# Performance work log

Measured on AMD Instinct MI355X. Metric: run time of the kernel, lower is better.

Reference implementation:

```python
import jax, jax.numpy as jnp
import numpy as np

B = 1024      # total windows (batch*windows_per_image)
W = 7         # window_size
T = W * W     # tokens per window = 49
C = 256       # scaled_emb_dim = emb_dim * 2**level
H = 8         # heads
D = C // H    # head_dim = 32
NUM_POS = 2 * W - 1


def _relative_pos():
    coords = np.arange(W)
    coords = np.stack(np.meshgrid(coords, coords, indexing='ij')).reshape(2, -1)
    rp = coords[:, :, None] - coords[:, None, :] + (W - 1)
    return jnp.asarray(rp, dtype=jnp.int32)  # (2, T, T)


def setup_inputs() -> dict:
    key = jax.random.key(0)
    ks = jax.random.split(key, 12)
    s = 0.02
    return {
        'x': jax.random.normal(ks[0], (B, T, C), dtype=jnp.float32),
        'relative_pos': _relative_pos(),
        'bias_table': jax.random.truncated_normal(ks[1], -2.0, 2.0, (H, NUM_POS, NUM_POS), dtype=jnp.float32) * s,
        'wq': jax.random.normal(ks[2], (C, H, D), dtype=jnp.float32) / np.sqrt(C),
        'bq': jnp.zeros((H, D), dtype=jnp.float32),
        'wk': jax.random.normal(ks[3], (C, H, D), dtype=jnp.float32) / np.sqrt(C),
        'bk': jnp.zeros((H, D), dtype=jnp.float32),
        'wv': jax.random.normal(ks[4], (C, H, D), dtype=jnp.float32) / np.sqrt(C),
        'bv': jnp.zeros((H, D), dtype=jnp.float32),
        'wo': jax.random.normal(ks[5], (H, D, C), dtype=jnp.float32) / np.sqrt(C),
        'bo': jnp.zeros((C,), dtype=jnp.float32),
        'dw': jax.random.normal(ks[6], (C, C), dtype=jnp.float32) / np.sqrt(C),
        'db': jnp.zeros((C,), dtype=jnp.float32),
    }


def reference(x, relative_pos, bias_table, wq, bq, wk, bk, wv, bv, wo, bo, dw, db):
    # QKV projections (flax DenseGeneral with bias)
    q = jnp.einsum('btc,chd->bthd', x, wq) + bq  # (B,T,H,D)
    k = jnp.einsum('btc,chd->bthd', x, wk) + bk
    v = jnp.einsum('btc,chd->bthd', x, wv) + bv

    # gathered relative position bias: (H, T, T)
    bias = bias_table[:, relative_pos[0], relative_pos[1]]

    # attention logits with query scaling (flax dot_product_attention)
    q = q / jnp.sqrt(jnp.asarray(D, dtype=q.dtype))
    logits = jnp.einsum('bqhd,bkhd->bhqk', q, k) + bias[None]
    attn = jax.nn.softmax(logits, axis=-1)

    out = jnp.einsum('bhqk,bkhd->bqhd', attn, v)
    y = jnp.einsum('bqhd,hdc->bqc', out, wo) + bo  # attention out projection
    y = jnp.einsum('btc,cf->btf', y, dw) + db      # trailing Dense(scaled_emb_dim)
    return y
```

## Files before the change

kernel.cpp:

```cpp
#include <hip/hip_runtime.h>
#include <stdint.h>

#define T 49
#define CCH 256
#define NH 8
#define DH 32

typedef __bf16 bf16x8 __attribute__((ext_vector_type(8)));
typedef float f32x4 __attribute__((ext_vector_type(4)));

static __device__ __forceinline__ unsigned short f2bf(float f){
  uint32_t u = __builtin_bit_cast(uint32_t, f);
  u = u + 0x7fffu + ((u >> 16) & 1u);
  return (unsigned short)(u >> 16);
}
static __device__ __forceinline__ float bf2f(unsigned short h){
  return __builtin_bit_cast(float, ((uint32_t)h) << 16);
}
static __device__ __forceinline__ f32x4 mfma16(bf16x8 a, bf16x8 b, f32x4 c){
  return __builtin_amdgcn_mfma_f32_16x16x32_bf16(a, b, c, 0, 0, 0);
}
#define SWZ(row) ((((row) & 7) << 4))


__global__ void prep_wqkvT(const float* __restrict__ wq, const float* __restrict__ wk,
                           const float* __restrict__ wv, unsigned short* __restrict__ out){
  int bk = blockIdx.x;
  int p = bk >> 8, kk = bk & 255;
  int n = threadIdx.x;
  const float* w = (p == 0) ? wq : (p == 1 ? wk : wv);
  float scl = (p == 0) ? 0.17677669529663687f : 1.0f;
  out[(size_t)(p * 256 + n) * 256 + kk] = f2bf(w[kk * 256 + n] * scl);
}

__global__ void prep_wodT(const float* __restrict__ wo, const float* __restrict__ dw,
                          unsigned short* __restrict__ out){
  int hd = blockIdx.x;
  int c = threadIdx.x;
  float s = 0.f;
  for (int cp = 0; cp < 256; ++cp) s = fmaf(wo[hd * 256 + cp], dw[cp * 256 + c], s);
  out[(size_t)c * 256 + hd] = f2bf(s);
}

__global__ void prep_misc(const int* __restrict__ rp, const float* __restrict__ btab,
                          const float* __restrict__ bq, const float* __restrict__ bk,
                          const float* __restrict__ bv, const float* __restrict__ bo,
                          const float* __restrict__ dwm, const float* __restrict__ db,
                          unsigned short* __restrict__ biasT, float* __restrict__ bqkv,
                          float* __restrict__ bod){
  int t = threadIdx.x;
  if (blockIdx.x == 0){
    for (int idx = t; idx < 768; idx += 256){
      int p = idx >> 8, n = idx & 255;
      float v = (p == 0) ? bq[n] * 0.17677669529663687f : (p == 1 ? bk[n] : bv[n]);
      bqkv[idx] = v;
    }
    float s = db[t];
    for (int cp = 0; cp < 256; ++cp) s = fmaf(bo[cp], dwm[cp * 256 + t], s);
    bod[t] = s;
  } else {
    int h = blockIdx.x - 1;
    for (int idx = t; idx < 4096; idx += 256){
      int j = idx >> 6, i = idx & 63;
      float v;
      if (j >= T) v = -1e30f;
      else if (i >= T) v = 0.f;
      else {
        int r0 = rp[i * 49 + j];
        int r1 = rp[2401 + i * 49 + j];
        v = btab[h * 169 + r0 * 13 + r1];
      }
      biasT[(size_t)(h * 64 + j) * 64 + i] = f2bf(v);
    }
  }
}

__launch_bounds__(512, 2)
__global__ void wmsa_main(const float* __restrict__ x,
                          const unsigned short* __restrict__ wqkvT,
                          const unsigned short* __restrict__ wodT,
                          const unsigned short* __restrict__ biasT,
                          const float* __restrict__ bqkv,
                          const float* __restrict__ bod,
                          float* __restrict__ y){
  __shared__ unsigned short xs[64 * 256];
  __shared__ unsigned short qs[8 * 64 * 40];
  __shared__ unsigned short ksh[8 * 64 * 40];
  __shared__ unsigned short vts[8 * 32 * 64];

  const int b    = blockIdx.x;
  const int tid  = threadIdx.x;
  const int h    = tid >> 6;
  const int lane = tid & 63;
  const int g    = lane >> 4;
  const int lo   = lane & 15;
  char* xs_c = (char*)xs;

  const float* xb = x + (size_t)b * T * CCH;
  for (int idx = tid; idx < 64 * 64; idx += 512){
    int row = idx >> 6, c4 = idx & 63;
    float4 v = make_float4(0.f, 0.f, 0.f, 0.f);
    if (row < T) v = reinterpret_cast<const float4*>(xb)[row * 64 + c4];
    uint32_t w0 = (uint32_t)f2bf(v.x) | ((uint32_t)f2bf(v.y) << 16);
    uint32_t w1 = (uint32_t)f2bf(v.z) | ((uint32_t)f2bf(v.w) << 16);
    *reinterpret_cast<uint2*>(xs_c + row * 512 + ((c4 * 8) ^ SWZ(row))) = make_uint2(w0, w1);
  }
  __syncthreads();

  f32x4 acc[4][6];
  #pragma unroll
  for (int mt = 0; mt < 4; ++mt)
    #pragma unroll
    for (int s = 0; s < 6; ++s) acc[mt][s] = f32x4{0.f, 0.f, 0.f, 0.f};

  for (int kt = 0; kt < 8; ++kt){
    bf16x8 a[4];
    #pragma unroll
    for (int mt = 0; mt < 4; ++mt){
      int row = 16 * mt + lo;
      a[mt] = *reinterpret_cast<const bf16x8*>(xs_c + row * 512 + ((kt * 64 + 16 * g) ^ SWZ(row)));
    }
    #pragma unroll
    for (int s = 0; s < 6; ++s){
      int p = s >> 1, nt = s & 1;
      int nrow = p * 256 + h * 32 + nt * 16 + lo;
      bf16x8 bfr = *reinterpret_cast<const bf16x8*>(wqkvT + (size_t)nrow * 256 + kt * 32 + 8 * g);
      #pragma unroll
      for (int mt = 0; mt < 4; ++mt) acc[mt][s] = mfma16(a[mt], bfr, acc[mt][s]);
    }
  }
  #pragma unroll
  for (int s = 0; s < 6; ++s){
    int p = s >> 1, nt = s & 1;
    int d = nt * 16 + lo;
    float bias = bqkv[p * 256 + h * 32 + d];
    #pragma unroll
    for (int mt = 0; mt < 4; ++mt){
      f32x4 t = acc[mt][s];
      if (p < 2){
        unsigned short* dst = (p == 0 ? qs : ksh) + h * 2560;
        #pragma unroll
        for (int r = 0; r < 4; ++r)
          dst[(16 * mt + 4 * g + r) * 40 + d] = f2bf(t[0 + r] + bias);
      } else {
        uint32_t w0 = (uint32_t)f2bf(t[0] + bias) | ((uint32_t)f2bf(t[1] + bias) << 16);
        uint32_t w1 = (uint32_t)f2bf(t[2] + bias) | ((uint32_t)f2bf(t[3] + bias) << 16);
        *reinterpret_cast<uint2*>((char*)vts + h * 4096 + d * 128 + ((mt * 32 + g * 8) ^ SWZ(d)))
            = make_uint2(w0, w1);
      }
    }
  }
  __syncthreads();

  const char* qb = (const char*)qs + h * 5120;
  const char* kb = (const char*)ksh + h * 5120;
  bf16x8 ak[4], bq_[4];
  #pragma unroll
  for (int tt = 0; tt < 4; ++tt){
    int row = 16 * tt + lo;
    ak[tt]  = *reinterpret_cast<const bf16x8*>(kb + row * 80 + 16 * g);
    bq_[tt] = *reinterpret_cast<const bf16x8*>(qb + row * 80 + 16 * g);
  }
  f32x4 lacc[4][4];
  #pragma unroll
  for (int mt = 0; mt < 4; ++mt)
    #pragma unroll
    for (int nt = 0; nt < 4; ++nt)
      lacc[mt][nt] = mfma16(ak[mt], bq_[nt], f32x4{0.f, 0.f, 0.f, 0.f});

  #pragma unroll
  for (int mt = 0; mt < 4; ++mt)
    #pragma unroll
    for (int nt = 0; nt < 4; ++nt)
      #pragma unroll
      for (int r = 0; r < 4; ++r){
        int j = 16 * mt + 4 * g + r, i = 16 * nt + lo;
        lacc[mt][nt][r] += bf2f(biasT[(size_t)(h * 64 + j) * 64 + i]);
      }

  float rs[4];
  uint32_t pw[4][4][2];
  #pragma unroll
  for (int nt = 0; nt < 4; ++nt){
    float m = -3.0e38f;
    #pragma unroll
    for (int mt = 0; mt < 4; ++mt)
      #pragma unroll
      for (int r = 0; r < 4; ++r) m = fmaxf(m, lacc[mt][nt][r]);
    m = fmaxf(m, __shfl_xor(m, 16, 64));
    m = fmaxf(m, __shfl_xor(m, 32, 64));
    float ssum = 0.f;
    #pragma unroll
    for (int mt = 0; mt < 4; ++mt)
      #pragma unroll
      for (int r = 0; r < 4; ++r){
        float pv = exp2f((lacc[mt][nt][r] - m) * 1.4426950408889634f);
        lacc[mt][nt][r] = pv;
        ssum += pv;
      }
    ssum += __shfl_xor(ssum, 16, 64);
    ssum += __shfl_xor(ssum, 32, 64);
    rs[nt] = 1.f / ssum;
    #pragma unroll
    for (int mt = 0; mt < 4; ++mt){
      pw[mt][nt][0] = (uint32_t)f2bf(lacc[mt][nt][0]) | ((uint32_t)f2bf(lacc[mt][nt][1]) << 16);
      pw[mt][nt][1] = (uint32_t)f2bf(lacc[mt][nt][2]) | ((uint32_t)f2bf(lacc[mt][nt][3]) << 16);
    }
  }

  const char* vb = (const char*)vts + h * 4096;
  f32x4 oacc[2][4];
  #pragma unroll
  for (int mt = 0; mt < 2; ++mt)
    #pragma unroll
    for (int nt = 0; nt < 4; ++nt) oacc[mt][nt] = f32x4{0.f, 0.f, 0.f, 0.f};

  const int src_lo = lo + 32 * (g & 1);
  const int src_hi = src_lo + 16;
  #pragma unroll
  for (int kt = 0; kt < 2; ++kt){
    bf16x8 av[2];
    #pragma unroll
    for (int mt = 0; mt < 2; ++mt){
      int row = 16 * mt + lo;
      av[mt] = *reinterpret_cast<const bf16x8*>(vb + row * 128 + ((kt * 64 + 16 * g) ^ SWZ(row)));
    }
    #pragma unroll
    for (int nt = 0; nt < 4; ++nt){
      uint32_t a0 = (uint32_t)__shfl((int)pw[2 * kt][nt][0], src_lo, 64);
      uint32_t a1 = (uint32_t)__shfl((int)pw[2 * kt][nt][1], src_lo, 64);
      uint32_t a2 = (uint32_t)__shfl((int)pw[2 * kt][nt][0], src_hi, 64);
      uint32_t a3 = (uint32_t)__shfl((int)pw[2 * kt][nt][1], src_hi, 64);
      uint32_t b0 = (uint32_t)__shfl((int)pw[2 * kt + 1][nt][0], src_lo, 64);
      uint32_t b1 = (uint32_t)__shfl((int)pw[2 * kt + 1][nt][1], src_lo, 64);
      uint32_t b2 = (uint32_t)__shfl((int)pw[2 * kt + 1][nt][0], src_hi, 64);
      uint32_t b3 = (uint32_t)__shfl((int)pw[2 * kt + 1][nt][1], src_hi, 64);
      uint4 fu = (g < 2) ? make_uint4(a0, a1, a2, a3) : make_uint4(b0, b1, b2, b3);
      bf16x8 pf = __builtin_bit_cast(bf16x8, fu);
      #pragma unroll
      for (int mt = 0; mt < 2; ++mt) oacc[mt][nt] = mfma16(av[mt], pf, oacc[mt][nt]);
    }
  }
  #pragma unroll
  for (int nt = 0; nt < 4; ++nt){
    int i = 16 * nt + lo;
    float r0 = rs[nt];
    #pragma unroll
    for (int mt = 0; mt < 2; ++mt){
      f32x4 t = oacc[mt][nt];
      uint32_t w0 = (uint32_t)f2bf(t[0] * r0) | ((uint32_t)f2bf(t[1] * r0) << 16);
      uint32_t w1 = (uint32_t)f2bf(t[2] * r0) | ((uint32_t)f2bf(t[3] * r0) << 16);
      *reinterpret_cast<uint2*>(xs_c + i * 512 + ((h * 64 + mt * 32 + g * 8) ^ SWZ(i)))
          = make_uint2(w0, w1);
    }
  }
  __syncthreads();

  f32x4 facc[4][2];
  #pragma unroll
  for (int mt = 0; mt < 4; ++mt)
    #pragma unroll
    for (int nt = 0; nt < 2; ++nt) facc[mt][nt] = f32x4{0.f, 0.f, 0.f, 0.f};

  for (int kt = 0; kt < 8; ++kt){
    bf16x8 a[4];
    #pragma unroll
    for (int mt = 0; mt < 4; ++mt){
      int row = 16 * mt + lo;
      a[mt] = *reinterpret_cast<const bf16x8*>(xs_c + row * 512 + ((kt * 64 + 16 * g) ^ SWZ(row)));
    }
    #pragma unroll
    for (int nt = 0; nt < 2; ++nt){
      int crow = h * 32 + nt * 16 + lo;
      bf16x8 bfr = *reinterpret_cast<const bf16x8*>(wodT + (size_t)crow * 256 + kt * 32 + 8 * g);
      #pragma unroll
      for (int mt = 0; mt < 4; ++mt) facc[mt][nt] = mfma16(a[mt], bfr, facc[mt][nt]);
    }
  }
  #pragma unroll
  for (int nt = 0; nt < 2; ++nt){
    int c = h * 32 + nt * 16 + lo;
    float bd = bod[c];
    #pragma unroll
    for (int mt = 0; mt < 4; ++mt)
      #pragma unroll
      for (int r = 0; r < 4; ++r){
        int i = 16 * mt + 4 * g + r;
        if (i < T) y[((size_t)b * T + i) * CCH + c] = facc[mt][nt][r] + bd;
      }
  }
}

extern "C" void kernel_launch(void* const* d_in, const int* in_sizes, int n_in,
                              void* d_out, int out_size, void* d_ws, size_t ws_size,
                              hipStream_t stream){
  const float* x    = (const float*)d_in[0];
  const int*   rp   = (const int*)d_in[1];
  const float* btab = (const float*)d_in[2];
  const float* wq   = (const float*)d_in[3];
  const float* bq   = (const float*)d_in[4];
  const float* wk   = (const float*)d_in[5];
  const float* bk   = (const float*)d_in[6];
  const float* wv   = (const float*)d_in[7];
  const float* bv   = (const float*)d_in[8];
  const float* wo   = (const float*)d_in[9];
  const float* bo   = (const float*)d_in[10];
  const float* dw   = (const float*)d_in[11];
  const float* db   = (const float*)d_in[12];
  float* y = (float*)d_out;

  char* ws = (char*)d_ws;
  unsigned short* wqkvT = (unsigned short*)(ws);
  unsigned short* wodT  = (unsigned short*)(ws + 393216);
  unsigned short* biasT = (unsigned short*)(ws + 524288);
  float* bqkv           = (float*)(ws + 589824);
  float* bod            = (float*)(ws + 592896);

  prep_wqkvT<<<768, 256, 0, stream>>>(wq, wk, wv, wqkvT);
  prep_wodT<<<256, 256, 0, stream>>>(wo, dw, wodT);
  prep_misc<<<9, 256, 0, stream>>>(rp, btab, bq, bk, bv, bo, dw, db, biasT, bqkv, bod);
  wmsa_main<<<1024, 512, 0, stream>>>(x, wqkvT, wodT, biasT, bqkv, bod, y);
}
```

Measured before the change: 163.5 us.

## Keep Q/K/V in registers via lane shuffles and drop attention LDS buffers

```diff
diff --git a/kernel.cpp b/kernel.cpp
--- a/kernel.cpp
+++ b/kernel.cpp
@@ -3,8 +3,6 @@
 
 #define T 49
 #define CCH 256
-#define NH 8
-#define DH 32
 
 typedef __bf16 bf16x8 __attribute__((ext_vector_type(8)));
 typedef float f32x4 __attribute__((ext_vector_type(4)));
@@ -17,10 +15,28 @@
 static __device__ __forceinline__ float bf2f(unsigned short h){
   return __builtin_bit_cast(float, ((uint32_t)h) << 16);
 }
+static __device__ __forceinline__ uint32_t pk2(float a, float b){
+  return (uint32_t)f2bf(a) | ((uint32_t)f2bf(b) << 16);
+}
 static __device__ __forceinline__ f32x4 mfma16(bf16x8 a, bf16x8 b, f32x4 c){
   return __builtin_amdgcn_mfma_f32_16x16x32_bf16(a, b, c, 0, 0, 0);
 }
 #define SWZ(row) ((((row) & 7) << 4))
+
+static __device__ __forceinline__ bf16x8 build_frag(uint32_t lo_w0, uint32_t lo_w1,
+                                                    uint32_t hi_w0, uint32_t hi_w1,
+                                                    int srcA, int srcB, bool use_hi){
+  uint32_t a0 = (uint32_t)__shfl((int)lo_w0, srcA, 64);
+  uint32_t c0 = (uint32_t)__shfl((int)hi_w0, srcA, 64);
+  uint32_t a1 = (uint32_t)__shfl((int)lo_w1, srcA, 64);
+  uint32_t c1 = (uint32_t)__shfl((int)hi_w1, srcA, 64);
+  uint32_t a2 = (uint32_t)__shfl((int)lo_w0, srcB, 64);
+  uint32_t c2 = (uint32_t)__shfl((int)hi_w0, srcB, 64);
+  uint32_t a3 = (uint32_t)__shfl((int)lo_w1, srcB, 64);
+  uint32_t c3 = (uint32_t)__shfl((int)hi_w1, srcB, 64);
+  uint4 u = use_hi ? make_uint4(c0, c1, c2, c3) : make_uint4(a0, a1, a2, a3);
+  return __builtin_bit_cast(bf16x8, u);
+}
 
 
 __global__ void prep_wqkvT(const float* __restrict__ wq, const float* __restrict__ wk,
@@ -46,7 +62,7 @@
                           const float* __restrict__ bq, const float* __restrict__ bk,
                           const float* __restrict__ bv, const float* __restrict__ bo,
                           const float* __restrict__ dwm, const float* __restrict__ db,
-                          unsigned short* __restrict__ biasT, float* __restrict__ bqkv,
+                          unsigned short* __restrict__ biasP, float* __restrict__ bqkv,
                           float* __restrict__ bod){
   int t = threadIdx.x;
   if (blockIdx.x == 0){
@@ -61,7 +77,13 @@
   } else {
     int h = blockIdx.x - 1;
     for (int idx = t; idx < 4096; idx += 256){
-      int j = idx >> 6, i = idx & 63;
+      int r  = idx & 3;
+      int lo = (idx >> 2) & 15;
+      int g  = (idx >> 6) & 3;
+      int nt = (idx >> 8) & 3;
+      int jt = idx >> 10;
+      int j = 16 * jt + 4 * g + r;
+      int i = 16 * nt + lo;
       float v;
       if (j >= T) v = -1e30f;
       else if (i >= T) v = 0.f;
@@ -70,23 +92,20 @@
         int r1 = rp[2401 + i * 49 + j];
         v = btab[h * 169 + r0 * 13 + r1];
       }
-      biasT[(size_t)(h * 64 + j) * 64 + i] = f2bf(v);
-    }
-  }
-}
-
-__launch_bounds__(512, 2)
+      biasP[h * 4096 + idx] = f2bf(v);
+    }
+  }
+}
+
+__launch_bounds__(512, 4)
 __global__ void wmsa_main(const float* __restrict__ x,
                           const unsigned short* __restrict__ wqkvT,
                           const unsigned short* __restrict__ wodT,
-                          const unsigned short* __restrict__ biasT,
+                          const unsigned short* __restrict__ biasP,
                           const float* __restrict__ bqkv,
                           const float* __restrict__ bod,
                           float* __restrict__ y){
   __shared__ unsigned short xs[64 * 256];
-  __shared__ unsigned short qs[8 * 64 * 40];
-  __shared__ unsigned short ksh[8 * 64 * 40];
-  __shared__ unsigned short vts[8 * 32 * 64];
 
   const int b    = blockIdx.x;
   const int tid  = threadIdx.x;
@@ -101,82 +120,123 @@
     int row = idx >> 6, c4 = idx & 63;
     float4 v = make_float4(0.f, 0.f, 0.f, 0.f);
     if (row < T) v = reinterpret_cast<const float4*>(xb)[row * 64 + c4];
-    uint32_t w0 = (uint32_t)f2bf(v.x) | ((uint32_t)f2bf(v.y) << 16);
-    uint32_t w1 = (uint32_t)f2bf(v.z) | ((uint32_t)f2bf(v.w) << 16);
+    uint32_t w0 = pk2(v.x, v.y);
+    uint32_t w1 = pk2(v.z, v.w);
     *reinterpret_cast<uint2*>(xs_c + row * 512 + ((c4 * 8) ^ SWZ(row))) = make_uint2(w0, w1);
   }
   __syncthreads();
 
-  f32x4 acc[4][6];
+  const int  srcA = lo + 16 * ((2 * g) & 3);
+  const int  srcB = lo + 16 * ((2 * g + 1) & 3);
+  const bool ghi  = (g >= 2);
+
+  f32x4 aq[2][4], akk[2][4];
+  #pragma unroll
+  for (int mt = 0; mt < 2; ++mt)
+    #pragma unroll
+    for (int nt = 0; nt < 4; ++nt){ aq[mt][nt] = f32x4{0,0,0,0}; akk[mt][nt] = f32x4{0,0,0,0}; }
+
+  for (int kt = 0; kt < 8; ++kt){
+    bf16x8 bx[4];
+    #pragma unroll
+    for (int nt = 0; nt < 4; ++nt){
+      int row = 16 * nt + lo;
+      bx[nt] = *reinterpret_cast<const bf16x8*>(xs_c + row * 512 + ((kt * 64 + 16 * g) ^ SWZ(row)));
+    }
+    #pragma unroll
+    for (int mt = 0; mt < 2; ++mt){
+      const bf16x8 wqf = *reinterpret_cast<const bf16x8*>(
+          wqkvT + (size_t)(h * 32 + 16 * mt + lo) * 256 + kt * 32 + 8 * g);
+      const bf16x8 wkf = *reinterpret_cast<const bf16x8*>(
+          wqkvT + (size_t)(256 + h * 32 + 16 * mt + lo) * 256 + kt * 32 + 8 * g);
+      #pragma unroll
+      for (int nt = 0; nt < 4; ++nt){
+        aq[mt][nt]  = mfma16(wqf, bx[nt], aq[mt][nt]);
+        akk[mt][nt] = mfma16(wkf, bx[nt], akk[mt][nt]);
+      }
+    }
+  }
+  uint32_t pq[2][4][2], pkk[2][4][2];
+  #pragma unroll
+  for (int mt = 0; mt < 2; ++mt){
+    const float4 b4q = *reinterpret_cast<const float4*>(bqkv + h * 32 + 16 * mt + 4 * g);
+    const float4 b4k = *reinterpret_cast<const float4*>(bqkv + 256 + h * 32 + 16 * mt + 4 * g);
+    #pragma unroll
+    for (int nt = 0; nt < 4; ++nt){
+      f32x4 tq = aq[mt][nt], tk = akk[mt][nt];
+      tq[0] += b4q.x; tq[1] += b4q.y; tq[2] += b4q.z; tq[3] += b4q.w;
+      tk[0] += b4k.x; tk[1] += b4k.y; tk[2] += b4k.z; tk[3] += b4k.w;
+      pq[mt][nt][0]  = pk2(tq[0], tq[1]); pq[mt][nt][1]  = pk2(tq[2], tq[3]);
+      pkk[mt][nt][0] = pk2(tk[0], tk[1]); pkk[mt][nt][1] = pk2(tk[2], tk[3]);
+    }
+  }
+  bf16x8 fq[4], fk[4];
+  #pragma unroll
+  for (int nt = 0; nt < 4; ++nt){
+    fq[nt] = build_frag(pq[0][nt][0],  pq[0][nt][1],  pq[1][nt][0],  pq[1][nt][1],  srcA, srcB, ghi);
+    fk[nt] = build_frag(pkk[0][nt][0], pkk[0][nt][1], pkk[1][nt][0], pkk[1][nt][1], srcA, srcB, ghi);
+  }
+
+  f32x4 avc[4][2];
   #pragma unroll
   for (int mt = 0; mt < 4; ++mt)
     #pragma unroll
-    for (int s = 0; s < 6; ++s) acc[mt][s] = f32x4{0.f, 0.f, 0.f, 0.f};
+    for (int nt = 0; nt < 2; ++nt) avc[mt][nt] = f32x4{0,0,0,0};
 
   for (int kt = 0; kt < 8; ++kt){
-    bf16x8 a[4];
+    bf16x8 ax[4];
     #pragma unroll
     for (int mt = 0; mt < 4; ++mt){
       int row = 16 * mt + lo;
-      a[mt] = *reinterpret_cast<const bf16x8*>(xs_c + row * 512 + ((kt * 64 + 16 * g) ^ SWZ(row)));
-    }
-    #pragma unroll
-    for (int s = 0; s < 6; ++s){
-      int p = s >> 1, nt = s & 1;
-      int nrow = p * 256 + h * 32 + nt * 16 + lo;
-      bf16x8 bfr = *reinterpret_cast<const bf16x8*>(wqkvT + (size_t)nrow * 256 + kt * 32 + 8 * g);
-      #pragma unroll
-      for (int mt = 0; mt < 4; ++mt) acc[mt][s] = mfma16(a[mt], bfr, acc[mt][s]);
-    }
-  }
-  #pragma unroll
-  for (int s = 0; s < 6; ++s){
-    int p = s >> 1, nt = s & 1;
-    int d = nt * 16 + lo;
-    float bias = bqkv[p * 256 + h * 32 + d];
+      ax[mt] = *reinterpret_cast<const bf16x8*>(xs_c + row * 512 + ((kt * 64 + 16 * g) ^ SWZ(row)));
+    }
+    #pragma unroll
+    for (int nt = 0; nt < 2; ++nt){
+      const bf16x8 wvf = *reinterpret_cast<const bf16x8*>(
+          wqkvT + (size_t)(512 + h * 32 + 16 * nt + lo) * 256 + kt * 32 + 8 * g);
+      #pragma unroll
+      for (int mt = 0; mt < 4; ++mt) avc[mt][nt] = mfma16(ax[mt], wvf, avc[mt][nt]);
+    }
+  }
+  __syncthreads();
+
+  uint32_t pv[4][2][2];
+  #pragma unroll
+  for (int nt = 0; nt < 2; ++nt){
+    const float bvs = bqkv[512 + h * 32 + 16 * nt + lo];
     #pragma unroll
     for (int mt = 0; mt < 4; ++mt){
-      f32x4 t = acc[mt][s];
-      if (p < 2){
-        unsigned short* dst = (p == 0 ? qs : ksh) + h * 2560;
-        #pragma unroll
-        for (int r = 0; r < 4; ++r)
-          dst[(16 * mt + 4 * g + r) * 40 + d] = f2bf(t[0 + r] + bias);
-      } else {
-        uint32_t w0 = (uint32_t)f2bf(t[0] + bias) | ((uint32_t)f2bf(t[1] + bias) << 16);
-        uint32_t w1 = (uint32_t)f2bf(t[2] + bias) | ((uint32_t)f2bf(t[3] + bias) << 16);
-        *reinterpret_cast<uint2*>((char*)vts + h * 4096 + d * 128 + ((mt * 32 + g * 8) ^ SWZ(d)))
-            = make_uint2(w0, w1);
-      }
-    }
-  }
-  __syncthreads();
-
-  const char* qb = (const char*)qs + h * 5120;
-  const char* kb = (const char*)ksh + h * 5120;
-  bf16x8 ak[4], bq_[4];
-  #pragma unroll
-  for (int tt = 0; tt < 4; ++tt){
-    int row = 16 * tt + lo;
-    ak[tt]  = *reinterpret_cast<const bf16x8*>(kb + row * 80 + 16 * g);
-    bq_[tt] = *reinterpret_cast<const bf16x8*>(qb + row * 80 + 16 * g);
-  }
+      f32x4 tv = avc[mt][nt];
+      tv[0] += bvs; tv[1] += bvs; tv[2] += bvs; tv[3] += bvs;
+      pv[mt][nt][0] = pk2(tv[0], tv[1]); pv[mt][nt][1] = pk2(tv[2], tv[3]);
+    }
+  }
+  bf16x8 av[2][2];
+  #pragma unroll
+  for (int dt = 0; dt < 2; ++dt)
+    #pragma unroll
+    for (int ktj = 0; ktj < 2; ++ktj)
+      av[dt][ktj] = build_frag(pv[2 * ktj][dt][0], pv[2 * ktj][dt][1],
+                               pv[2 * ktj + 1][dt][0], pv[2 * ktj + 1][dt][1], srcA, srcB, ghi);
+
   f32x4 lacc[4][4];
   #pragma unroll
-  for (int mt = 0; mt < 4; ++mt)
+  for (int jt = 0; jt < 4; ++jt)
     #pragma unroll
     for (int nt = 0; nt < 4; ++nt)
-      lacc[mt][nt] = mfma16(ak[mt], bq_[nt], f32x4{0.f, 0.f, 0.f, 0.f});
-
-  #pragma unroll
-  for (int mt = 0; mt < 4; ++mt)
-    #pragma unroll
-    for (int nt = 0; nt < 4; ++nt)
-      #pragma unroll
-      for (int r = 0; r < 4; ++r){
-        int j = 16 * mt + 4 * g + r, i = 16 * nt + lo;
-        lacc[mt][nt][r] += bf2f(biasT[(size_t)(h * 64 + j) * 64 + i]);
-      }
+      lacc[jt][nt] = mfma16(fk[jt], fq[nt], f32x4{0,0,0,0});
+
+  #pragma unroll
+  for (int jt = 0; jt < 4; ++jt)
+    #pragma unroll
+    for (int nt = 0; nt < 4; ++nt){
+      const uint2 bb = *reinterpret_cast<const uint2*>(
+          biasP + h * 4096 + jt * 1024 + nt * 256 + (g * 16 + lo) * 4);
+      lacc[jt][nt][0] += bf2f((unsigned short)(bb.x & 0xffff));
+      lacc[jt][nt][1] += bf2f((unsigned short)(bb.x >> 16));
+      lacc[jt][nt][2] += bf2f((unsigned short)(bb.y & 0xffff));
+      lacc[jt][nt][3] += bf2f((unsigned short)(bb.y >> 16));
+    }
 
   float rs[4];
   uint32_t pw[4][4][2];
@@ -184,73 +244,56 @@
   for (int nt = 0; nt < 4; ++nt){
     float m = -3.0e38f;
     #pragma unroll
-    for (int mt = 0; mt < 4; ++mt)
-      #pragma unroll
-      for (int r = 0; r < 4; ++r) m = fmaxf(m, lacc[mt][nt][r]);
+    for (int jt = 0; jt < 4; ++jt)
+      #pragma unroll
+      for (int r = 0; r < 4; ++r) m = fmaxf(m, lacc[jt][nt][r]);
     m = fmaxf(m, __shfl_xor(m, 16, 64));
     m = fmaxf(m, __shfl_xor(m, 32, 64));
     float ssum = 0.f;
     #pragma unroll
-    for (int mt = 0; mt < 4; ++mt)
+    for (int jt = 0; jt < 4; ++jt)
       #pragma unroll
       for (int r = 0; r < 4; ++r){
-        float pv = exp2f((lacc[mt][nt][r] - m) * 1.4426950408889634f);
-        lacc[mt][nt][r] = pv;
-        ssum += pv;
+        float pvv = exp2f((lacc[jt][nt][r] - m) * 1.4426950408889634f);
+        lacc[jt][nt][r] = pvv;
+        ssum += pvv;
       }
     ssum += __shfl_xor(ssum, 16, 64);
     ssum += __shfl_xor(ssum, 32, 64);
     rs[nt] = 1.f / ssum;
     #pragma unroll
-    for (int mt = 0; mt < 4; ++mt){
-      pw[mt][nt][0] = (uint32_t)f2bf(lacc[mt][nt][0]) | ((uint32_t)f2bf(lacc[mt][nt][1]) << 16);
-      pw[mt][nt][1] = (uint32_t)f2bf(lacc[mt][nt][2]) | ((uint32_t)f2bf(lacc[mt][nt][3]) << 16);
-    }
-  }
-
-  const char* vb = (const char*)vts + h * 4096;
+    for (int jt = 0; jt < 4; ++jt){
+      pw[jt][nt][0] = pk2(lacc[jt][nt][0], lacc[jt][nt][1]);
+      pw[jt][nt][1] = pk2(lacc[jt][nt][2], lacc[jt][nt][3]);
+    }
+  }
+
   f32x4 oacc[2][4];
   #pragma unroll
-  for (int mt = 0; mt < 2; ++mt)
-    #pragma unroll
-    for (int nt = 0; nt < 4; ++nt) oacc[mt][nt] = f32x4{0.f, 0.f, 0.f, 0.f};
-
-  const int src_lo = lo + 32 * (g & 1);
-  const int src_hi = src_lo + 16;
-  #pragma unroll
-  for (int kt = 0; kt < 2; ++kt){
-    bf16x8 av[2];
-    #pragma unroll
-    for (int mt = 0; mt < 2; ++mt){
-      int row = 16 * mt + lo;
-      av[mt] = *reinterpret_cast<const bf16x8*>(vb + row * 128 + ((kt * 64 + 16 * g) ^ SWZ(row)));
-    }
+  for (int dt = 0; dt < 2; ++dt)
+    #pragma unroll
+    for (int nt = 0; nt < 4; ++nt) oacc[dt][nt] = f32x4{0,0,0,0};
+
+  #pragma unroll
+  for (int ktj = 0; ktj < 2; ++ktj)
     #pragma unroll
     for (int nt = 0; nt < 4; ++nt){
-      uint32_t a0 = (uint32_t)__shfl((int)pw[2 * kt][nt][0], src_lo, 64);
-      uint32_t a1 = (uint32_t)__shfl((int)pw[2 * kt][nt][1], src_lo, 64);
-      uint32_t a2 = (uint32_t)__shfl((int)pw[2 * kt][nt][0], src_hi, 64);
-      uint32_t a3 = (uint32_t)__shfl((int)pw[2 * kt][nt][1], src_hi, 64);
-      uint32_t b0 = (uint32_t)__shfl((int)pw[2 * kt + 1][nt][0], src_lo, 64);
-      uint32_t b1 = (uint32_t)__shfl((int)pw[2 * kt + 1][nt][1], src_lo, 64);
-      uint32_t b2 = (uint32_t)__shfl((int)pw[2 * kt + 1][nt][0], src_hi, 64);
-      uint32_t b3 = (uint32_t)__shfl((int)pw[2 * kt + 1][nt][1], src_hi, 64);
-      uint4 fu = (g < 2) ? make_uint4(a0, a1, a2, a3) : make_uint4(b0, b1, b2, b3);
-      bf16x8 pf = __builtin_bit_cast(bf16x8, fu);
-      #pragma unroll
-      for (int mt = 0; mt < 2; ++mt) oacc[mt][nt] = mfma16(av[mt], pf, oacc[mt][nt]);
-    }
-  }
+      bf16x8 pf = build_frag(pw[2 * ktj][nt][0], pw[2 * ktj][nt][1],
+                             pw[2 * ktj + 1][nt][0], pw[2 * ktj + 1][nt][1], srcA, srcB, ghi);
+      #pragma unroll
+      for (int dt = 0; dt < 2; ++dt) oacc[dt][nt] = mfma16(av[dt][ktj], pf, oacc[dt][nt]);
+    }
+
   #pragma unroll
   for (int nt = 0; nt < 4; ++nt){
     int i = 16 * nt + lo;
     float r0 = rs[nt];
     #pragma unroll
-    for (int mt = 0; mt < 2; ++mt){
-      f32x4 t = oacc[mt][nt];
-      uint32_t w0 = (uint32_t)f2bf(t[0] * r0) | ((uint32_t)f2bf(t[1] * r0) << 16);
-      uint32_t w1 = (uint32_t)f2bf(t[2] * r0) | ((uint32_t)f2bf(t[3] * r0) << 16);
-      *reinterpret_cast<uint2*>(xs_c + i * 512 + ((h * 64 + mt * 32 + g * 8) ^ SWZ(i)))
+    for (int dt = 0; dt < 2; ++dt){
+      f32x4 t = oacc[dt][nt];
+      uint32_t w0 = pk2(t[0] * r0, t[1] * r0);
+      uint32_t w1 = pk2(t[2] * r0, t[3] * r0);
+      *reinterpret_cast<uint2*>(xs_c + i * 512 + ((h * 64 + dt * 32 + g * 8) ^ SWZ(i)))
           = make_uint2(w0, w1);
     }
   }
@@ -260,7 +303,7 @@
   #pragma unroll
   for (int mt = 0; mt < 4; ++mt)
     #pragma unroll
-    for (int nt = 0; nt < 2; ++nt) facc[mt][nt] = f32x4{0.f, 0.f, 0.f, 0.f};
+    for (int nt = 0; nt < 2; ++nt) facc[mt][nt] = f32x4{0,0,0,0};
 
   for (int kt = 0; kt < 8; ++kt){
     bf16x8 a[4];
@@ -272,7 +315,7 @@
     #pragma unroll
     for (int nt = 0; nt < 2; ++nt){
       int crow = h * 32 + nt * 16 + lo;
-      bf16x8 bfr = *reinterpret_cast<const bf16x8*>(wodT + (size_t)crow * 256 + kt * 32 + 8 * g);
+      const bf16x8 bfr = *reinterpret_cast<const bf16x8*>(wodT + (size_t)crow * 256 + kt * 32 + 8 * g);
       #pragma unroll
       for (int mt = 0; mt < 4; ++mt) facc[mt][nt] = mfma16(a[mt], bfr, facc[mt][nt]);
     }
@@ -312,12 +355,12 @@
   char* ws = (char*)d_ws;
   unsigned short* wqkvT = (unsigned short*)(ws);
   unsigned short* wodT  = (unsigned short*)(ws + 393216);
-  unsigned short* biasT = (unsigned short*)(ws + 524288);
+  unsigned short* biasP = (unsigned short*)(ws + 524288);
   float* bqkv           = (float*)(ws + 589824);
   float* bod            = (float*)(ws + 592896);
 
   prep_wqkvT<<<768, 256, 0, stream>>>(wq, wk, wv, wqkvT);
   prep_wodT<<<256, 256, 0, stream>>>(wo, dw, wodT);
-  prep_misc<<<9, 256, 0, stream>>>(rp, btab, bq, bk, bv, bo, dw, db, biasT, bqkv, bod);
-  wmsa_main<<<1024, 512, 0, stream>>>(x, wqkvT, wodT, biasT, bqkv, bod, y);
-}
+  prep_misc<<<9, 256, 0, stream>>>(rp, btab, bq, bk, bv, bo, dw, db, biasP, bqkv, bod);
+  wmsa_main<<<1024, 512, 0, stream>>>(x, wqkvT, wodT, biasP, bqkv, bod, y);
+}
```

New measurement: 215.8 us. 1.32x slower.
